# Kernel tuning notes

Measured on AMD Instinct MI355X. Metric: run time of the kernel, lower is better.

The kernel has to match this reference:

```python
import jax, jax.numpy as jnp
import numpy as np

B, S, D, H, DFF = 2, 2048, 768, 12, 2048
DK = D // H
EPS = 1e-6


def setup_inputs() -> dict:
    key = jax.random.key(0)
    ks = jax.random.split(key, 16)
    sd = 0.02
    inp = {
        "x": jax.random.normal(ks[0], (B, S, D), jnp.float32),
        "mask": jnp.ones((B, 1, S), jnp.int32),
        "Wq": jax.random.normal(ks[1], (D, D), jnp.float32) * sd,
        "bq": jnp.zeros((D,), jnp.float32),
        "Wk": jax.random.normal(ks[2], (D, D), jnp.float32) * sd,
        "bk": jnp.zeros((D,), jnp.float32),
        "Wv": jax.random.normal(ks[3], (D, D), jnp.float32) * sd,
        "bv": jnp.zeros((D,), jnp.float32),
        "Wo": jax.random.normal(ks[4], (D, D), jnp.float32) * sd,
        "bo": jnp.zeros((D,), jnp.float32),
        "W1": jax.random.normal(ks[5], (DFF, D), jnp.float32) * sd,
        "b1": jnp.zeros((DFF,), jnp.float32),
        "W2": jax.random.normal(ks[6], (D, DFF), jnp.float32) * sd,
        "b2": jnp.zeros((D,), jnp.float32),
        "alpha": jnp.ones((D,), jnp.float32),
        "beta": jnp.zeros((D,), jnp.float32),
    }
    return inp


def _norm(x, alpha, beta):
    # Matches torch Norm: std with Bessel correction (ddof=1), eps added to std.
    mu = jnp.mean(x, axis=-1, keepdims=True)
    sd = jnp.std(x, axis=-1, keepdims=True, ddof=1)
    return alpha * (x - mu) / (sd + EPS) + beta


def reference(x, mask, Wq, bq, Wk, bk, Wv, bv, Wo, bo, W1, b1, W2, b2, alpha, beta):
    # --- pre-norm MHA block ---
    n = _norm(x, alpha, beta)
    q = (n @ Wq.T + bq).reshape(B, S, H, DK).transpose(0, 2, 1, 3)  # [B,H,S,DK]
    k = (n @ Wk.T + bk).reshape(B, S, H, DK).transpose(0, 2, 1, 3)
    v = (n @ Wv.T + bv).reshape(B, S, H, DK).transpose(0, 2, 1, 3)
    scores = jnp.einsum("bhqd,bhkd->bhqk", q, k) / jnp.sqrt(jnp.float32(DK))
    # mask: [B,1,S] -> unsqueeze(1) -> [B,1,1,S], broadcast over heads & query rows
    scores = jnp.where(mask[:, None, :, :] == 0, jnp.float32(-1e9), scores)
    attn = jax.nn.softmax(scores, axis=-1)
    # dropout is identity in eval mode
    ctx = jnp.einsum("bhqk,bhkd->bhqd", attn, v)  # [B,H,S,DK]
    concat = ctx.transpose(0, 2, 1, 3).reshape(B, S, D)
    x = x + (concat @ Wo.T + bo)
    # --- pre-norm FFN block (same shared Norm params) ---
    n2 = _norm(x, alpha, beta)
    h = jax.nn.relu(n2 @ W1.T + b1)
    x = x + (h @ W2.T + b2)
    return x
```

## Files before the change

### kernel.cpp

```cpp
#include <hip/hip_runtime.h>

#define SS   2048
#define DD   768
#define HH   12
#define DFFF 2048
#define BSR  4096
#define QKV_LD 2304

typedef __attribute__((ext_vector_type(8))) short bf16x8;
typedef __attribute__((ext_vector_type(4))) float f32x4;

__device__ __forceinline__ unsigned short f2b(float f) {
  union { float f; unsigned u; } x; x.f = f;
  unsigned r = (x.u + 0x7FFFu + ((x.u >> 16) & 1u)) >> 16;
  return (unsigned short)r;
}

__device__ __forceinline__ unsigned cvtpk(float lo, float hi) {
  unsigned r;
  asm("v_cvt_pk_bf16_f32 %0, %1, %2" : "=v"(r) : "v"(lo), "v"(hi));
  return r;
}

__device__ __forceinline__ void gload_lds16(const void* g, void* l) {
  __builtin_amdgcn_global_load_lds(
      (const __attribute__((address_space(1))) unsigned int*)g,
      (__attribute__((address_space(3))) unsigned int*)l,
      16, 0, 0);
}

__device__ __forceinline__ unsigned lds_u32(const void* p) {
  return (unsigned)(unsigned long long)p;
}

__device__ __forceinline__ void ln_row(const float* __restrict__ xr,
                                       const float* __restrict__ alpha,
                                       const float* __restrict__ beta,
                                       unsigned short* __restrict__ orow, int lane) {
  float4 v[3];
#pragma unroll
  for (int g = 0; g < 3; ++g) v[g] = *(const float4*)&xr[lane * 12 + g * 4];
  float sum = 0.f;
#pragma unroll
  for (int g = 0; g < 3; ++g) sum += v[g].x + v[g].y + v[g].z + v[g].w;
#pragma unroll
  for (int off = 1; off < 64; off <<= 1) sum += __shfl_xor(sum, off);
  float mu = sum * (1.0f / 768.0f);
  float ss = 0.f;
#pragma unroll
  for (int g = 0; g < 3; ++g) {
    float a0 = v[g].x - mu, a1 = v[g].y - mu, a2 = v[g].z - mu, a3 = v[g].w - mu;
    ss += a0 * a0 + a1 * a1 + a2 * a2 + a3 * a3;
  }
#pragma unroll
  for (int off = 1; off < 64; off <<= 1) ss += __shfl_xor(ss, off);
  float sd = sqrtf(ss * (1.0f / 767.0f));
  float inv = 1.0f / (sd + 1e-6f);
#pragma unroll
  for (int g = 0; g < 3; ++g) {
    float4 al = *(const float4*)&alpha[lane * 12 + g * 4];
    float4 be = *(const float4*)&beta[lane * 12 + g * 4];
    uint2 pk;
    pk.x = cvtpk(al.x * (v[g].x - mu) * inv + be.x, al.y * (v[g].y - mu) * inv + be.y);
    pk.y = cvtpk(al.z * (v[g].z - mu) * inv + be.z, al.w * (v[g].w - mu) * inv + be.w);
    *(uint2*)&orow[lane * 12 + g * 4] = pk;
  }
}

__global__ __launch_bounds__(256) void pre_k(const float* __restrict__ Wq,
                                             const float* __restrict__ Wk,
                                             const float* __restrict__ Wv,
                                             const float* __restrict__ Wo,
                                             const float* __restrict__ W1,
                                             const float* __restrict__ W2,
                                             const float* __restrict__ bq,
                                             const float* __restrict__ bk,
                                             const float* __restrict__ bv,
                                             const float* __restrict__ x,
                                             const float* __restrict__ alpha,
                                             const float* __restrict__ beta,
                                             unsigned short* __restrict__ wqkv,
                                             unsigned short* __restrict__ wo_b,
                                             unsigned short* __restrict__ w1_b,
                                             unsigned short* __restrict__ w2_b,
                                             float* __restrict__ bqkv,
                                             unsigned short* __restrict__ n_b) {
  const int blk = blockIdx.x;
  const float* src;
  unsigned short* dst;
  long off;
  if (blk < 1728) {
    int r = blk / 576;
    src = r == 0 ? Wq : r == 1 ? Wk : Wv;
    dst = wqkv + (long)r * 589824;
    off = (long)(blk - r * 576) * 1024 + threadIdx.x * 4;
  } else if (blk < 2304) {
    src = Wo; dst = wo_b; off = (long)(blk - 1728) * 1024 + threadIdx.x * 4;
  } else if (blk < 3840) {
    src = W1; dst = w1_b; off = (long)(blk - 2304) * 1024 + threadIdx.x * 4;
  } else if (blk < 5376) {
    src = W2; dst = w2_b; off = (long)(blk - 3840) * 1024 + threadIdx.x * 4;
  } else if (blk == 5376) {
    for (int k = threadIdx.x; k < 2304; k += 256)
      bqkv[k] = k < 768 ? bq[k] : k < 1536 ? bk[k - 768] : bv[k - 1536];
    return;
  } else {
    int row = (blk - 5377) * 4 + (threadIdx.x >> 6);
    ln_row(x + (long)row * DD, alpha, beta, n_b + (long)row * DD, threadIdx.x & 63);
    return;
  }
  float4 v = *(const float4*)&src[off];
  uint2 pk;
  pk.x = cvtpk(v.x, v.y);
  pk.y = cvtpk(v.z, v.w);
  *(uint2*)&dst[off] = pk;
}

__global__ __launch_bounds__(256) void layernorm_k(const float* __restrict__ x,
                                                   const float* __restrict__ alpha,
                                                   const float* __restrict__ beta,
                                                   unsigned short* __restrict__ outb) {
  int row = blockIdx.x * 4 + (threadIdx.x >> 6);
  ln_row(x + (long)row * DD, alpha, beta, outb + (long)row * DD, threadIdx.x & 63);
}

template <int BM, int BN, bool RELU, bool RES, bool OUTB, bool QSC>
__global__ __launch_bounds__(256, (BM == 64 || BN == 64) ? 4 : 3)
void gemm_bt(const unsigned short* __restrict__ A,
             const unsigned short* __restrict__ W,
             const float* __restrict__ bias,
             const float* __restrict__ res,
             void* __restrict__ outp,
             int M, int N, int K) {
  __shared__ __align__(16) unsigned short As[BM * 64];
  __shared__ __align__(16) unsigned short Bs[BN * 64];
  constexpr int MF = BM / 32;
  constexpr int NF = BN / 32;
  const int t = threadIdx.x;
  const int lane = t & 63;
  const int w = t >> 6;
  const int wr = w >> 1, wc = w & 1;
  const int l15 = lane & 15, l4 = lane >> 4;
  const int nwg = gridDim.x * gridDim.y;
  const int lin = blockIdx.y * gridDim.x + blockIdx.x;
  const int u2 = (lin & 7) * (nwg >> 3) + (lin >> 3);
  const long brow = (long)(u2 / gridDim.x) * BM;
  const long bcol = (long)(u2 % gridDim.x) * BN;
  f32x4 acc[MF][NF] = {};
  const int r0 = t >> 3;
  const int c8s = (((t & 7) ^ (r0 & 7)) & 7) * 8;
  const int rd_swz = (l15 & 7) << 4;

  for (int k0 = 0; k0 < K; k0 += 64) {
    __syncthreads();
#pragma unroll
    for (int p = 0; p < BM / 32; ++p)
      gload_lds16(&A[(brow + p * 32 + r0) * (long)K + k0 + c8s],
                  (char*)As + p * 4096 + w * 1024);
#pragma unroll
    for (int p = 0; p < BN / 32; ++p)
      gload_lds16(&W[(bcol + p * 32 + r0) * (long)K + k0 + c8s],
                  (char*)Bs + p * 4096 + w * 1024);
    __syncthreads();
#pragma unroll
    for (int ks = 0; ks < 2; ++ks) {
      bf16x8 a[MF], b[NF];
#pragma unroll
      for (int m = 0; m < MF; ++m)
        a[m] = *(const bf16x8*)((const char*)As +
                                (wr * (BM / 2) + m * 16 + l15) * 128 +
                                ((ks * 64 + l4 * 16) ^ rd_swz));
#pragma unroll
      for (int n = 0; n < NF; ++n)
        b[n] = *(const bf16x8*)((const char*)Bs +
                                (wc * (BN / 2) + n * 16 + l15) * 128 +
                                ((ks * 64 + l4 * 16) ^ rd_swz));
#pragma unroll
      for (int m = 0; m < MF; ++m)
#pragma unroll
        for (int n = 0; n < NF; ++n)
          acc[m][n] = __builtin_amdgcn_mfma_f32_16x16x32_bf16(a[m], b[n], acc[m][n], 0, 0, 0);
    }
  }
#pragma unroll
  for (int n = 0; n < NF; ++n) {
    const long col = bcol + wc * (BN / 2) + n * 16 + l15;
    const float bv = bias[col];
    const float sc = (QSC && col < 768) ? 0.18033688f : 1.0f;
#pragma unroll
    for (int m = 0; m < MF; ++m) {
      const long row0 = brow + wr * (BM / 2) + m * 16 + l4 * 4;
#pragma unroll
      for (int r = 0; r < 4; ++r) {
        float v = acc[m][n][r] + bv;
        if (RELU) v = fmaxf(v, 0.0f);
        if (QSC) v *= sc;
        long o = (row0 + r) * (long)N + col;
        if (RES) v += res[o];
        if (OUTB) ((unsigned short*)outp)[o] = f2b(v);
        else ((float*)outp)[o] = v;
      }
    }
  }
}

__global__ __launch_bounds__(256, 4) void attn_kernel(const unsigned short* __restrict__ qkv,
                                                      const int* __restrict__ mask,
                                                      unsigned short* __restrict__ ctx) {
  __shared__ __align__(16) unsigned short Ks[2][64 * 64];
  __shared__ __align__(16) unsigned short Vt[2][64 * 64];
  const int t = threadIdx.x, lane = t & 63, w = t >> 6;
  const int l15 = lane & 15, l4 = lane >> 4;
  const int u = (blockIdx.x & 7) * 96 + (blockIdx.x >> 3);
  const int qt = u & 31;
  const int h = (u >> 5) % 12;
  const int b = u / 384;
  const long rowB = (long)b * SS;

  unsigned bm;
  {
    int* tfl = (int*)&Vt[0][0];
    const int* mb = &mask[b * SS + t * 8];
    int4 a0 = *(const int4*)mb;
    int4 a1 = *(const int4*)(mb + 4);
    int allv = (a0.x && a0.y && a0.z && a0.w && a1.x && a1.y && a1.z && a1.w) ? 1 : 0;
    allv &= __shfl_xor(allv, 1);
    allv &= __shfl_xor(allv, 2);
    allv &= __shfl_xor(allv, 4);
    if ((t & 7) == 0) tfl[t >> 3] = allv;
    __syncthreads();
    int vv = (lane < 32) ? tfl[lane] : 1;
    bm = (unsigned)__ballot(vv);
    __syncthreads();
  }

  bf16x8 aq[2];
#pragma unroll
  for (int ks = 0; ks < 2; ++ks)
    aq[ks] = *(const bf16x8*)&qkv[(rowB + qt * 64 + w * 16 + l15) * QKV_LD +
                                  h * 64 + ks * 32 + l4 * 8];

  const int krow = w * 8 + (lane >> 3);
  const int kdo = (((lane & 7) ^ (lane >> 3)) & 7) << 3;
  const unsigned short* kgbase = &qkv[(rowB + krow) * QKV_LD + 768 + h * 64 + kdo];
  const int kread_swz = (l15 & 7) << 4;

  const unsigned short* vsrc[2];
#pragma unroll
  for (int p = 0; p < 2; ++p) {
    int X = p * 4096 + w * 1024 + lane * 16;
    int d_blk = X >> 11;
    int rem = X & 2047;
    int k_blk = rem >> 7;
    int krw = (rem >> 5) & 3;
    int c = (rem >> 4) & 1;
    int vkey = k_blk * 4 + krw;
    int vd0 = d_blk * 16 + c * 8;
    vsrc[p] = &qkv[(rowB + vkey) * QKV_LD + 1536 + h * 64 + vd0];
  }
  const unsigned vtrl = (unsigned)(l15 * 2 + l4 * 128);
  const unsigned vt0 = lds_u32(&Vt[0][0]) + vtrl;
  const unsigned vt1 = lds_u32(&Vt[1][0]) + vtrl;

  union { unsigned uu[4]; bf16x8 b8; } vone;
  vone.uu[0] = vone.uu[1] = vone.uu[2] = vone.uu[3] = 0x3F803F80u;

  f32x4 o[4] = {};
  f32x4 o4 = {};
  float mrun = -1e30f;

#pragma unroll
  for (int p = 0; p < 2; ++p)
    gload_lds16(kgbase + (long)p * 32 * QKV_LD, (char*)Ks[0] + p * 4096 + w * 1024);
#pragma unroll
  for (int p = 0; p < 2; ++p)
    gload_lds16(vsrc[p], (char*)Vt[0] + p * 4096 + w * 1024);
  __syncthreads();

  for (int kb = 0; kb < 32; ++kb) {
    const int bi = kb & 1;
    const char* Kc = (const char*)Ks[bi];
    const unsigned vaddr = bi ? vt1 : vt0;
    if (kb < 31) {
#pragma unroll
      for (int p = 0; p < 2; ++p)
        gload_lds16(kgbase + ((long)(kb + 1) * 64 + p * 32) * QKV_LD,
                    (char*)Ks[bi ^ 1] + p * 4096 + w * 1024);
#pragma unroll
      for (int p = 0; p < 2; ++p)
        gload_lds16(vsrc[p] + (long)(kb + 1) * 64 * QKV_LD,
                    (char*)Vt[bi ^ 1] + p * 4096 + w * 1024);
    }
    f32x4 s[4] = {};
    __builtin_amdgcn_s_setprio(1);
#pragma unroll
    for (int ks = 0; ks < 2; ++ks)
#pragma unroll
      for (int cg = 0; cg < 4; ++cg) {
        bf16x8 ak = *(const bf16x8*)(Kc + (cg * 16 + l15) * 128 +
                                     ((ks * 64 + l4 * 16) ^ kread_swz));
        s[cg] = __builtin_amdgcn_mfma_f32_16x16x32_bf16(ak, aq[ks], s[cg], 0, 0, 0);
      }
    __builtin_amdgcn_s_setprio(0);
    if (__builtin_expect(!((bm >> kb) & 1), 0)) {
      const int* mb2 = &mask[b * SS + kb * 64 + l4 * 4];
#pragma unroll
      for (int cg = 0; cg < 4; ++cg) {
        int4 mm = *(const int4*)(mb2 + cg * 16);
        int mi[4] = {mm.x, mm.y, mm.z, mm.w};
#pragma unroll
        for (int r = 0; r < 4; ++r) s[cg][r] += mi[r] ? 0.f : -1.44269504e9f;
      }
    }
    float t0 = fmaxf(fmaxf(s[0][0], s[0][1]), s[0][2]);
    float t1 = fmaxf(fmaxf(s[0][3], s[1][0]), s[1][1]);
    float t2 = fmaxf(fmaxf(s[1][2], s[1][3]), s[2][0]);
    float t3 = fmaxf(fmaxf(s[2][1], s[2][2]), s[2][3]);
    float t4 = fmaxf(fmaxf(s[3][0], s[3][1]), s[3][2]);
    float t5 = fmaxf(fmaxf(t0, t1), t2);
    float t6 = fmaxf(fmaxf(t3, t4), s[3][3]);
    float pmax = fmaxf(t5, t6);
    pmax = fmaxf(pmax, __shfl_xor(pmax, 16));
    pmax = fmaxf(pmax, __shfl_xor(pmax, 32));
    if (!__all(pmax <= mrun + 8.0f)) {
      float mnew = fmaxf(mrun, pmax);
      float fac = __builtin_amdgcn_exp2f(mrun - mnew);
#pragma unroll
      for (int mg = 0; mg < 4; ++mg)
#pragma unroll
        for (int r = 0; r < 4; ++r) o[mg][r] *= fac;
#pragma unroll
      for (int r = 0; r < 4; ++r) o4[r] *= fac;
      mrun = mnew;
    }
#pragma unroll
    for (int cg = 0; cg < 4; ++cg)
#pragma unroll
      for (int r = 0; r < 4; ++r)
        s[cg][r] = __builtin_amdgcn_exp2f(s[cg][r] - mrun);
    __builtin_amdgcn_s_setprio(1);
#pragma unroll
    for (int ks = 0; ks < 2; ++ks) {
      union { unsigned uu[4]; bf16x8 b8; } bp;
      bp.uu[0] = cvtpk(s[2 * ks][0], s[2 * ks][1]);
      bp.uu[1] = cvtpk(s[2 * ks][2], s[2 * ks][3]);
      bp.uu[2] = cvtpk(s[2 * ks + 1][0], s[2 * ks + 1][1]);
      bp.uu[3] = cvtpk(s[2 * ks + 1][2], s[2 * ks + 1][3]);
      uint2 q0, q1, q2, q3, q4, q5, q6, q7;
      if (ks == 0) {
        asm volatile(
            "ds_read_b64_tr_b16 %0, %8 offset:0\n\t"
            "ds_read_b64_tr_b16 %1, %8 offset:512\n\t"
            "ds_read_b64_tr_b16 %2, %8 offset:2048\n\t"
            "ds_read_b64_tr_b16 %3, %8 offset:2560\n\t"
            "ds_read_b64_tr_b16 %4, %8 offset:4096\n\t"
            "ds_read_b64_tr_b16 %5, %8 offset:4608\n\t"
            "ds_read_b64_tr_b16 %6, %8 offset:6144\n\t"
            "ds_read_b64_tr_b16 %7, %8 offset:6656\n\t"
            "s_waitcnt lgkmcnt(0)"
            : "=&v"(q0), "=&v"(q1), "=&v"(q2), "=&v"(q3),
              "=&v"(q4), "=&v"(q5), "=&v"(q6), "=&v"(q7)
            : "v"(vaddr));
      } else {
        asm volatile(
            "ds_read_b64_tr_b16 %0, %8 offset:1024\n\t"
            "ds_read_b64_tr_b16 %1, %8 offset:1536\n\t"
            "ds_read_b64_tr_b16 %2, %8 offset:3072\n\t"
            "ds_read_b64_tr_b16 %3, %8 offset:3584\n\t"
            "ds_read_b64_tr_b16 %4, %8 offset:5120\n\t"
            "ds_read_b64_tr_b16 %5, %8 offset:5632\n\t"
            "ds_read_b64_tr_b16 %6, %8 offset:7168\n\t"
            "ds_read_b64_tr_b16 %7, %8 offset:7680\n\t"
            "s_waitcnt lgkmcnt(0)"
            : "=&v"(q0), "=&v"(q1), "=&v"(q2), "=&v"(q3),
              "=&v"(q4), "=&v"(q5), "=&v"(q6), "=&v"(q7)
            : "v"(vaddr));
      }
      union { uint2 u2[2]; bf16x8 b8; } av0, av1, av2, av3;
      av0.u2[0] = q0; av0.u2[1] = q1;
      av1.u2[0] = q2; av1.u2[1] = q3;
      av2.u2[0] = q4; av2.u2[1] = q5;
      av3.u2[0] = q6; av3.u2[1] = q7;
      o[0] = __builtin_amdgcn_mfma_f32_16x16x32_bf16(av0.b8, bp.b8, o[0], 0, 0, 0);
      o[1] = __builtin_amdgcn_mfma_f32_16x16x32_bf16(av1.b8, bp.b8, o[1], 0, 0, 0);
      o[2] = __builtin_amdgcn_mfma_f32_16x16x32_bf16(av2.b8, bp.b8, o[2], 0, 0, 0);
      o[3] = __builtin_amdgcn_mfma_f32_16x16x32_bf16(av3.b8, bp.b8, o[3], 0, 0, 0);
      o4 = __builtin_amdgcn_mfma_f32_16x16x32_bf16(vone.b8, bp.b8, o4, 0, 0, 0);
    }
    __builtin_amdgcn_s_setprio(0);
    __syncthreads();
  }
  const float inv = 1.0f / o4[0];
  const long obase = (rowB + qt * 64 + w * 16 + l15) * DD + h * 64 + l4 * 4;
#pragma unroll
  for (int mg = 0; mg < 4; ++mg) {
    *(unsigned*)&ctx[obase + mg * 16] = cvtpk(o[mg][0] * inv, o[mg][1] * inv);
    *(unsigned*)&ctx[obase + mg * 16 + 2] = cvtpk(o[mg][2] * inv, o[mg][3] * inv);
  }
}

static const size_t OFF_WQKV = 0;
static const size_t OFF_WO = 3538944;
static const size_t OFF_W1 = 4718592;
static const size_t OFF_W2 = 7864320;
static const size_t OFF_BQKV = 11010048;
static const size_t OFF_N = 11019264;
static const size_t OFF_QKV = 17310720;
static const size_t OFF_CTX = 36185088;
static const size_t OFF_X1 = 42476544;

extern "C" void kernel_launch(void* const* d_in, const int* in_sizes, int n_in,
                              void* d_out, int out_size, void* d_ws, size_t ws_size,
                              hipStream_t stream) {
  (void)in_sizes; (void)n_in; (void)out_size; (void)ws_size;
  const float* x = (const float*)d_in[0];
  const int* mask = (const int*)d_in[1];
  const float* Wq = (const float*)d_in[2];
  const float* bq = (const float*)d_in[3];
  const float* Wk = (const float*)d_in[4];
  const float* bk = (const float*)d_in[5];
  const float* Wv = (const float*)d_in[6];
  const float* bv = (const float*)d_in[7];
  const float* Wo = (const float*)d_in[8];
  const float* bo = (const float*)d_in[9];
  const float* W1 = (const float*)d_in[10];
  const float* b1 = (const float*)d_in[11];
  const float* W2 = (const float*)d_in[12];
  const float* b2 = (const float*)d_in[13];
  const float* alpha = (const float*)d_in[14];
  const float* beta = (const float*)d_in[15];

  char* ws = (char*)d_ws;
  unsigned short* wqkv = (unsigned short*)(ws + OFF_WQKV);
  unsigned short* wo_b = (unsigned short*)(ws + OFF_WO);
  unsigned short* w1_b = (unsigned short*)(ws + OFF_W1);
  unsigned short* w2_b = (unsigned short*)(ws + OFF_W2);
  float* bqkv = (float*)(ws + OFF_BQKV);
  unsigned short* n_b = (unsigned short*)(ws + OFF_N);
  unsigned short* qkv_b = (unsigned short*)(ws + OFF_QKV);
  unsigned short* h_b = qkv_b;
  unsigned short* ctx_b = (unsigned short*)(ws + OFF_CTX);
  float* x1_f = (float*)(ws + OFF_X1);
  float* out_f = (float*)d_out;

  pre_k<<<6401, 256, 0, stream>>>(Wq, Wk, Wv, Wo, W1, W2, bq, bk, bv,
                                  x, alpha, beta, wqkv, wo_b, w1_b, w2_b, bqkv, n_b);
  gemm_bt<128, 128, false, false, true, true><<<dim3(18, 32), 256, 0, stream>>>(
      n_b, wqkv, bqkv, nullptr, qkv_b, BSR, QKV_LD, DD);
  attn_kernel<<<768, 256, 0, stream>>>(qkv_b, mask, ctx_b);
  gemm_bt<64, 64, false, true, false, false><<<dim3(12, 64), 256, 0, stream>>>(
      ctx_b, wo_b, bo, x, x1_f, BSR, DD, DD);
  layernorm_k<<<1024, 256, 0, stream>>>(x1_f, alpha, beta, n_b);
  gemm_bt<64, 128, true, false, true, false><<<dim3(16, 64), 256, 0, stream>>>(
      n_b, w1_b, b1, nullptr, h_b, BSR, DFFF, DD);
  gemm_bt<64, 64, false, true, false, false><<<dim3(12, 64), 256, 0, stream>>>(
      h_b, w2_b, b2, x1_f, out_f, BSR, DD, DFFF);
}
```

Baseline: 139.2 us.

## Software-pipeline attention: overlap next QK^T MFMA with current softmax and PV

Restructures the attention inner loop so the QK^T scores for block i+1 are computed while the softmax and PV product for block i proceed. V gets a triple-buffered LDS ring, and K loads now run two blocks ahead. The aim is to hide exp and reduction latency behind MFMA work and to cut stalls at the barrier. The cost is more LDS and registers, so launch bounds drop from 4 to 3 blocks per SIMD, which reduces occupancy.

```diff
diff --git a/kernel.cpp b/kernel.cpp
--- a/kernel.cpp
+++ b/kernel.cpp
@@ -204,11 +204,11 @@
   }
 }
 
-__global__ __launch_bounds__(256, 4) void attn_kernel(const unsigned short* __restrict__ qkv,
+__global__ __launch_bounds__(256, 3) void attn_kernel(const unsigned short* __restrict__ qkv,
                                                       const int* __restrict__ mask,
                                                       unsigned short* __restrict__ ctx) {
   __shared__ __align__(16) unsigned short Ks[2][64 * 64];
-  __shared__ __align__(16) unsigned short Vt[2][64 * 64];
+  __shared__ __align__(16) unsigned short Vt[3][64 * 64];
   const int t = threadIdx.x, lane = t & 63, w = t >> 6;
   const int l15 = lane & 15, l4 = lane >> 4;
   const int u = (blockIdx.x & 7) * 96 + (blockIdx.x >> 3);
@@ -259,8 +259,14 @@
     vsrc[p] = &qkv[(rowB + vkey) * QKV_LD + 1536 + h * 64 + vd0];
   }
   const unsigned vtrl = (unsigned)(l15 * 2 + l4 * 128);
-  const unsigned vt0 = lds_u32(&Vt[0][0]) + vtrl;
-  const unsigned vt1 = lds_u32(&Vt[1][0]) + vtrl;
+  unsigned vad0 = lds_u32(&Vt[0][0]) + vtrl;
+  unsigned vad1 = lds_u32(&Vt[1][0]) + vtrl;
+  unsigned vad2 = lds_u32(&Vt[2][0]) + vtrl;
+  char* vdst0 = (char*)&Vt[2][0];
+  char* vdst1 = (char*)&Vt[0][0];
+  char* vdst2 = (char*)&Vt[1][0];
+  const char* kread = (const char*)&Ks[1][0];
+  char* kdst = (char*)&Ks[0][0];
 
   union { unsigned uu[4]; bf16x8 b8; } vone;
   vone.uu[0] = vone.uu[1] = vone.uu[2] = vone.uu[3] = 0x3F803F80u;
@@ -268,84 +274,97 @@
   f32x4 o[4] = {};
   f32x4 o4 = {};
   float mrun = -1e30f;
+  f32x4 sp[4];
+
+#define QK_INTO(dst, kbase)                                                     \
+  { __builtin_amdgcn_s_setprio(1);                                             \
+    _Pragma("unroll") for (int ks = 0; ks < 2; ++ks)                           \
+    _Pragma("unroll") for (int cg = 0; cg < 4; ++cg) {                         \
+      bf16x8 ak = *(const bf16x8*)((kbase) + (cg * 16 + l15) * 128 +           \
+                                   ((ks * 64 + l4 * 16) ^ kread_swz));         \
+      dst[cg] = __builtin_amdgcn_mfma_f32_16x16x32_bf16(ak, aq[ks], dst[cg], 0, 0, 0); \
+    }                                                                           \
+    __builtin_amdgcn_s_setprio(0); }
+
+#define MASK_APPLY(dst, kb)                                                     \
+  if (__builtin_expect(!((bm >> (kb)) & 1), 0)) {                              \
+    const int* mb2 = &mask[b * SS + (kb) * 64 + l4 * 4];                       \
+    _Pragma("unroll") for (int cg = 0; cg < 4; ++cg) {                         \
+      int4 mm = *(const int4*)(mb2 + cg * 16);                                 \
+      int mi[4] = {mm.x, mm.y, mm.z, mm.w};                                    \
+      _Pragma("unroll") for (int r = 0; r < 4; ++r)                            \
+        dst[cg][r] += mi[r] ? 0.f : -1.44269504e9f;                            \
+    } }
 
 #pragma unroll
   for (int p = 0; p < 2; ++p)
-    gload_lds16(kgbase + (long)p * 32 * QKV_LD, (char*)Ks[0] + p * 4096 + w * 1024);
+    gload_lds16(kgbase + (long)p * 32 * QKV_LD, (char*)&Ks[0][0] + p * 4096 + w * 1024);
 #pragma unroll
   for (int p = 0; p < 2; ++p)
-    gload_lds16(vsrc[p], (char*)Vt[0] + p * 4096 + w * 1024);
+    gload_lds16(vsrc[p], (char*)&Vt[0][0] + p * 4096 + w * 1024);
   __syncthreads();
-
-  for (int kb = 0; kb < 32; ++kb) {
-    const int bi = kb & 1;
-    const char* Kc = (const char*)Ks[bi];
-    const unsigned vaddr = bi ? vt1 : vt0;
-    if (kb < 31) {
+#pragma unroll
+  for (int p = 0; p < 2; ++p)
+    gload_lds16(kgbase + ((long)64 + p * 32) * QKV_LD, (char*)&Ks[1][0] + p * 4096 + w * 1024);
+#pragma unroll
+  for (int p = 0; p < 2; ++p)
+    gload_lds16(vsrc[p] + (long)64 * QKV_LD, (char*)&Vt[1][0] + p * 4096 + w * 1024);
+#pragma unroll
+  for (int cg = 0; cg < 4; ++cg) sp[cg] = f32x4{0.f, 0.f, 0.f, 0.f};
+  QK_INTO(sp, (const char*)&Ks[0][0]);
+  MASK_APPLY(sp, 0);
+
+  for (int i = 0; i < 31; ++i) {
+    __syncthreads();
+    if (i < 30) {
 #pragma unroll
       for (int p = 0; p < 2; ++p)
-        gload_lds16(kgbase + ((long)(kb + 1) * 64 + p * 32) * QKV_LD,
-                    (char*)Ks[bi ^ 1] + p * 4096 + w * 1024);
+        gload_lds16(kgbase + ((long)(i + 2) * 64 + p * 32) * QKV_LD,
+                    kdst + p * 4096 + w * 1024);
 #pragma unroll
       for (int p = 0; p < 2; ++p)
-        gload_lds16(vsrc[p] + (long)(kb + 1) * 64 * QKV_LD,
-                    (char*)Vt[bi ^ 1] + p * 4096 + w * 1024);
-    }
-    f32x4 s[4] = {};
-    __builtin_amdgcn_s_setprio(1);
-#pragma unroll
-    for (int ks = 0; ks < 2; ++ks)
-#pragma unroll
-      for (int cg = 0; cg < 4; ++cg) {
-        bf16x8 ak = *(const bf16x8*)(Kc + (cg * 16 + l15) * 128 +
-                                     ((ks * 64 + l4 * 16) ^ kread_swz));
-        s[cg] = __builtin_amdgcn_mfma_f32_16x16x32_bf16(ak, aq[ks], s[cg], 0, 0, 0);
+        gload_lds16(vsrc[p] + (long)(i + 2) * 64 * QKV_LD,
+                    vdst0 + p * 4096 + w * 1024);
+    }
+    f32x4 sc[4] = {};
+    QK_INTO(sc, kread);
+    MASK_APPLY(sc, i + 1);
+    {
+      float t0 = fmaxf(fmaxf(sp[0][0], sp[0][1]), sp[0][2]);
+      float t1 = fmaxf(fmaxf(sp[0][3], sp[1][0]), sp[1][1]);
+      float t2 = fmaxf(fmaxf(sp[1][2], sp[1][3]), sp[2][0]);
+      float t3 = fmaxf(fmaxf(sp[2][1], sp[2][2]), sp[2][3]);
+      float t4 = fmaxf(fmaxf(sp[3][0], sp[3][1]), sp[3][2]);
+      float t5 = fmaxf(fmaxf(t0, t1), t2);
+      float t6 = fmaxf(fmaxf(t3, t4), sp[3][3]);
+      float pmax = fmaxf(t5, t6);
+      pmax = fmaxf(pmax, __shfl_xor(pmax, 16));
+      pmax = fmaxf(pmax, __shfl_xor(pmax, 32));
+      if (!__all(pmax <= mrun + 8.0f)) {
+        float mnew = fmaxf(mrun, pmax);
+        float fac = __builtin_amdgcn_exp2f(mrun - mnew);
+#pragma unroll
+        for (int mg = 0; mg < 4; ++mg)
+#pragma unroll
+          for (int r = 0; r < 4; ++r) o[mg][r] *= fac;
+#pragma unroll
+        for (int r = 0; r < 4; ++r) o4[r] *= fac;
+        mrun = mnew;
       }
-    __builtin_amdgcn_s_setprio(0);
-    if (__builtin_expect(!((bm >> kb) & 1), 0)) {
-      const int* mb2 = &mask[b * SS + kb * 64 + l4 * 4];
-#pragma unroll
-      for (int cg = 0; cg < 4; ++cg) {
-        int4 mm = *(const int4*)(mb2 + cg * 16);
-        int mi[4] = {mm.x, mm.y, mm.z, mm.w};
-#pragma unroll
-        for (int r = 0; r < 4; ++r) s[cg][r] += mi[r] ? 0.f : -1.44269504e9f;
-      }
-    }
-    float t0 = fmaxf(fmaxf(s[0][0], s[0][1]), s[0][2]);
-    float t1 = fmaxf(fmaxf(s[0][3], s[1][0]), s[1][1]);
-    float t2 = fmaxf(fmaxf(s[1][2], s[1][3]), s[2][0]);
-    float t3 = fmaxf(fmaxf(s[2][1], s[2][2]), s[2][3]);
-    float t4 = fmaxf(fmaxf(s[3][0], s[3][1]), s[3][2]);
-    float t5 = fmaxf(fmaxf(t0, t1), t2);
-    float t6 = fmaxf(fmaxf(t3, t4), s[3][3]);
-    float pmax = fmaxf(t5, t6);
-    pmax = fmaxf(pmax, __shfl_xor(pmax, 16));
-    pmax = fmaxf(pmax, __shfl_xor(pmax, 32));
-    if (!__all(pmax <= mrun + 8.0f)) {
-      float mnew = fmaxf(mrun, pmax);
-      float fac = __builtin_amdgcn_exp2f(mrun - mnew);
-#pragma unroll
-      for (int mg = 0; mg < 4; ++mg)
-#pragma unroll
-        for (int r = 0; r < 4; ++r) o[mg][r] *= fac;
-#pragma unroll
-      for (int r = 0; r < 4; ++r) o4[r] *= fac;
-      mrun = mnew;
-    }
-#pragma unroll
-    for (int cg = 0; cg < 4; ++cg)
-#pragma unroll
-      for (int r = 0; r < 4; ++r)
-        s[cg][r] = __builtin_amdgcn_exp2f(s[cg][r] - mrun);
+#pragma unroll
+      for (int cg = 0; cg < 4; ++cg)
+#pragma unroll
+        for (int r = 0; r < 4; ++r)
+          sp[cg][r] = __builtin_amdgcn_exp2f(sp[cg][r] - mrun);
+    }
     __builtin_amdgcn_s_setprio(1);
 #pragma unroll
     for (int ks = 0; ks < 2; ++ks) {
       union { unsigned uu[4]; bf16x8 b8; } bp;
-      bp.uu[0] = cvtpk(s[2 * ks][0], s[2 * ks][1]);
-      bp.uu[1] = cvtpk(s[2 * ks][2], s[2 * ks][3]);
-      bp.uu[2] = cvtpk(s[2 * ks + 1][0], s[2 * ks + 1][1]);
-      bp.uu[3] = cvtpk(s[2 * ks + 1][2], s[2 * ks + 1][3]);
+      bp.uu[0] = cvtpk(sp[2 * ks][0], sp[2 * ks][1]);
+      bp.uu[1] = cvtpk(sp[2 * ks][2], sp[2 * ks][3]);
+      bp.uu[2] = cvtpk(sp[2 * ks + 1][0], sp[2 * ks + 1][1]);
+      bp.uu[3] = cvtpk(sp[2 * ks + 1][2], sp[2 * ks + 1][3]);
       uint2 q0, q1, q2, q3, q4, q5, q6, q7;
       if (ks == 0) {
         asm volatile(
@@ -360,7 +379,7 @@
             "s_waitcnt lgkmcnt(0)"
             : "=&v"(q0), "=&v"(q1), "=&v"(q2), "=&v"(q3),
               "=&v"(q4), "=&v"(q5), "=&v"(q6), "=&v"(q7)
-            : "v"(vaddr));
+            : "v"(vad0));
       } else {
         asm volatile(
             "ds_read_b64_tr_b16 %0, %8 offset:1024\n\t"
@@ -374,7 +393,7 @@
             "s_waitcnt lgkmcnt(0)"
             : "=&v"(q0), "=&v"(q1), "=&v"(q2), "=&v"(q3),
               "=&v"(q4), "=&v"(q5), "=&v"(q6), "=&v"(q7)
-            : "v"(vaddr));
+            : "v"(vad0));
       }
       union { uint2 u2[2]; bf16x8 b8; } av0, av1, av2, av3;
       av0.u2[0] = q0; av0.u2[1] = q1;
@@ -388,8 +407,92 @@
       o4 = __builtin_amdgcn_mfma_f32_16x16x32_bf16(vone.b8, bp.b8, o4, 0, 0, 0);
     }
     __builtin_amdgcn_s_setprio(0);
-    __syncthreads();
-  }
+#pragma unroll
+    for (int cg = 0; cg < 4; ++cg) sp[cg] = sc[cg];
+    { const char* tk = kread; kread = kdst; kdst = (char*)tk; }
+    { unsigned tv = vad0; vad0 = vad1; vad1 = vad2; vad2 = tv; }
+    { char* td = vdst0; vdst0 = vdst1; vdst1 = vdst2; vdst2 = td; }
+  }
+
+  {
+    float t0 = fmaxf(fmaxf(sp[0][0], sp[0][1]), sp[0][2]);
+    float t1 = fmaxf(fmaxf(sp[0][3], sp[1][0]), sp[1][1]);
+    float t2 = fmaxf(fmaxf(sp[1][2], sp[1][3]), sp[2][0]);
+    float t3 = fmaxf(fmaxf(sp[2][1], sp[2][2]), sp[2][3]);
+    float t4 = fmaxf(fmaxf(sp[3][0], sp[3][1]), sp[3][2]);
+    float t5 = fmaxf(fmaxf(t0, t1), t2);
+    float t6 = fmaxf(fmaxf(t3, t4), sp[3][3]);
+    float pmax = fmaxf(t5, t6);
+    pmax = fmaxf(pmax, __shfl_xor(pmax, 16));
+    pmax = fmaxf(pmax, __shfl_xor(pmax, 32));
+    if (!__all(pmax <= mrun + 8.0f)) {
+      float mnew = fmaxf(mrun, pmax);
+      float fac = __builtin_amdgcn_exp2f(mrun - mnew);
+#pragma unroll
+      for (int mg = 0; mg < 4; ++mg)
+#pragma unroll
+        for (int r = 0; r < 4; ++r) o[mg][r] *= fac;
+#pragma unroll
+      for (int r = 0; r < 4; ++r) o4[r] *= fac;
+      mrun = mnew;
+    }
+#pragma unroll
+    for (int cg = 0; cg < 4; ++cg)
+#pragma unroll
+      for (int r = 0; r < 4; ++r)
+        sp[cg][r] = __builtin_amdgcn_exp2f(sp[cg][r] - mrun);
+#pragma unroll
+    for (int ks = 0; ks < 2; ++ks) {
+      union { unsigned uu[4]; bf16x8 b8; } bp;
+      bp.uu[0] = cvtpk(sp[2 * ks][0], sp[2 * ks][1]);
+      bp.uu[1] = cvtpk(sp[2 * ks][2], sp[2 * ks][3]);
+      bp.uu[2] = cvtpk(sp[2 * ks + 1][0], sp[2 * ks + 1][1]);
+      bp.uu[3] = cvtpk(sp[2 * ks + 1][2], sp[2 * ks + 1][3]);
+      uint2 q0, q1, q2, q3, q4, q5, q6, q7;
+      if (ks == 0) {
+        asm volatile(
+            "ds_read_b64_tr_b16 %0, %8 offset:0\n\t"
+            "ds_read_b64_tr_b16 %1, %8 offset:512\n\t"
+            "ds_read_b64_tr_b16 %2, %8 offset:2048\n\t"
+            "ds_read_b64_tr_b16 %3, %8 offset:2560\n\t"
+            "ds_read_b64_tr_b16 %4, %8 offset:4096\n\t"
+            "ds_read_b64_tr_b16 %5, %8 offset:4608\n\t"
+            "ds_read_b64_tr_b16 %6, %8 offset:6144\n\t"
+            "ds_read_b64_tr_b16 %7, %8 offset:6656\n\t"
+            "s_waitcnt lgkmcnt(0)"
+            : "=&v"(q0), "=&v"(q1), "=&v"(q2), "=&v"(q3),
+              "=&v"(q4), "=&v"(q5), "=&v"(q6), "=&v"(q7)
+            : "v"(vad0));
+      } else {
+        asm volatile(
+            "ds_read_b64_tr_b16 %0, %8 offset:1024\n\t"
+            "ds_read_b64_tr_b16 %1, %8 offset:1536\n\t"
+            "ds_read_b64_tr_b16 %2, %8 offset:3072\n\t"
+            "ds_read_b64_tr_b16 %3, %8 offset:3584\n\t"
+            "ds_read_b64_tr_b16 %4, %8 offset:5120\n\t"
+            "ds_read_b64_tr_b16 %5, %8 offset:5632\n\t"
+            "ds_read_b64_tr_b16 %6, %8 offset:7168\n\t"
+            "ds_read_b64_tr_b16 %7, %8 offset:7680\n\t"
+            "s_waitcnt lgkmcnt(0)"
+            : "=&v"(q0), "=&v"(q1), "=&v"(q2), "=&v"(q3),
+              "=&v"(q4), "=&v"(q5), "=&v"(q6), "=&v"(q7)
+            : "v"(vad0));
+      }
+      union { uint2 u2[2]; bf16x8 b8; } av0, av1, av2, av3;
+      av0.u2[0] = q0; av0.u2[1] = q1;
+      av1.u2[0] = q2; av1.u2[1] = q3;
+      av2.u2[0] = q4; av2.u2[1] = q5;
+      av3.u2[0] = q6; av3.u2[1] = q7;
+      o[0] = __builtin_amdgcn_mfma_f32_16x16x32_bf16(av0.b8, bp.b8, o[0], 0, 0, 0);
+      o[1] = __builtin_amdgcn_mfma_f32_16x16x32_bf16(av1.b8, bp.b8, o[1], 0, 0, 0);
+      o[2] = __builtin_amdgcn_mfma_f32_16x16x32_bf16(av2.b8, bp.b8, o[2], 0, 0, 0);
+      o[3] = __builtin_amdgcn_mfma_f32_16x16x32_bf16(av3.b8, bp.b8, o[3], 0, 0, 0);
+      o4 = __builtin_amdgcn_mfma_f32_16x16x32_bf16(vone.b8, bp.b8, o4, 0, 0, 0);
+    }
+  }
+#undef QK_INTO
+#undef MASK_APPLY
+
   const float inv = 1.0f / o4[0];
   const long obase = (rowB + qt * 64 + w * 16 + l15) * DD + h * 64 + l4 * 4;
 #pragma unroll
```

After: 135.3 us. 1.03x faster.
